# Optimization experiments

Hardware: AMD Instinct MI355X
Metric: run time of the kernel (lower is better)

## Reference

```python
import jax, jax.numpy as jnp
import numpy as np

B, Hdim, Wdim, C, NH, WS, SS = 8, 112, 112, 128, 4, 7, 3
N = WS * WS  # tokens per window


def _build_attn_mask(H, W, ws, ss):
    # standard Swin shifted-window mask: (nW, N, N) with 0 / -100
    img_mask = np.zeros((1, H, W, 1), dtype=np.float32)
    cnt = 0
    for h in (slice(0, -ws), slice(-ws, -ss), slice(-ss, None)):
        for w in (slice(0, -ws), slice(-ws, -ss), slice(-ss, None)):
            img_mask[:, h, w, :] = cnt
            cnt += 1
    mw = img_mask.reshape(1, H // ws, ws, W // ws, ws, 1)
    mw = mw.transpose(0, 1, 3, 2, 4, 5).reshape(-1, ws * ws)  # (nW, N)
    attn_mask = mw[:, None, :] - mw[:, :, None]
    return np.where(attn_mask != 0, np.float32(-100.0), np.float32(0.0))


def _rel_pos_index(ws):
    coords = np.stack(np.meshgrid(np.arange(ws), np.arange(ws), indexing='ij'))  # 2,ws,ws
    cf = coords.reshape(2, -1)
    rel = cf[:, :, None] - cf[:, None, :]  # 2,N,N
    rel = rel.transpose(1, 2, 0)
    rel[:, :, 0] += ws - 1
    rel[:, :, 1] += ws - 1
    rel[:, :, 0] *= 2 * ws - 1
    return rel.sum(-1).astype(np.int32)  # (N, N)


def setup_inputs() -> dict:
    key = jax.random.key(0)
    ks = jax.random.split(key, 6)
    x = jax.random.normal(ks[0], (B, Hdim * Wdim, C), dtype=jnp.float32)
    mask_matrix = jnp.asarray(_build_attn_mask(Hdim, Wdim, WS, SS))  # (256,49,49)
    s = 0.02
    qkv_w = jax.random.normal(ks[1], (3 * C, C), dtype=jnp.float32) * s
    qkv_b = jnp.zeros((3 * C,), dtype=jnp.float32)
    proj_w = jax.random.normal(ks[2], (C, C), dtype=jnp.float32) * s
    proj_b = jnp.zeros((C,), dtype=jnp.float32)
    rpb_table = jax.random.normal(ks[3], ((2 * WS - 1) ** 2, NH), dtype=jnp.float32) * s
    rel_index = jnp.asarray(_rel_pos_index(WS))
    return dict(x=x, mask_matrix=mask_matrix, qkv_w=qkv_w, qkv_b=qkv_b,
                proj_w=proj_w, proj_b=proj_b, rpb_table=rpb_table,
                rel_index=rel_index, H=Hdim, W=Wdim,
                window_size=WS, shift_size=SS, num_heads=NH)


def reference(x, mask_matrix, qkv_w, qkv_b, proj_w, proj_b, rpb_table,
              rel_index, H, W, window_size, shift_size, num_heads):
    Bb, L, Cc = x.shape
    ws, ss, nh = window_size, shift_size, num_heads
    hd = Cc // nh
    n = ws * ws
    x = x.reshape(Bb, H, W, Cc)
    if ss > 0:
        x = jnp.roll(x, shift=(-ss, -ss), axis=(1, 2))
    # window partition -> (Bb*nW, n, C)
    nWh, nWw = H // ws, W // ws
    xw = x.reshape(Bb, nWh, ws, nWw, ws, Cc).transpose(0, 1, 3, 2, 4, 5)
    xw = xw.reshape(-1, n, Cc)
    Bw = xw.shape[0]
    # qkv
    qkv = xw @ qkv_w.T + qkv_b  # (Bw, n, 3C)
    qkv = qkv.reshape(Bw, n, 3, nh, hd).transpose(2, 0, 3, 1, 4)
    q, k, v = qkv[0], qkv[1], qkv[2]  # (Bw, nh, n, hd)
    attn = jnp.einsum('bhnd,bhmd->bhnm', q * (hd ** -0.5), k)
    bias = rpb_table[rel_index.reshape(-1)].reshape(n, n, nh).transpose(2, 0, 1)
    attn = attn + bias[None]
    if ss > 0:
        nW = mask_matrix.shape[0]
        attn = attn.reshape(Bw // nW, nW, nh, n, n) + mask_matrix[None, :, None]
        attn = attn.reshape(Bw, nh, n, n)
    attn = jax.nn.softmax(attn, axis=-1)
    out = jnp.einsum('bhnm,bhmd->bhnd', attn, v)
    out = out.transpose(0, 2, 1, 3).reshape(Bw, n, Cc)
    out = out @ proj_w.T + proj_b
    # window reverse
    out = out.reshape(Bb, nWh, nWw, ws, ws, Cc).transpose(0, 1, 3, 2, 4, 5)
    out = out.reshape(Bb, H, W, Cc)
    if ss > 0:
        out = jnp.roll(out, shift=(ss, ss), axis=(1, 2))
    return out.reshape(Bb, H * W, Cc)
```

## Files before the change

### kernel.cpp

```cpp
#include <hip/hip_runtime.h>
#include <hip/hip_bf16.h>

typedef unsigned short u16;
typedef unsigned int   u32;
typedef __attribute__((ext_vector_type(8))) short bf16x8;
typedef __attribute__((ext_vector_type(4))) float f32x4;

__device__ __forceinline__ float bflo(u32 w) { return __uint_as_float(w << 16); }
__device__ __forceinline__ float bfhi(u32 w) { return __uint_as_float(w & 0xffff0000u); }
__device__ __forceinline__ u16 f2bf(float f) {
    u32 u = __float_as_uint(f);
    return (u16)((u + 0x7fffu + ((u >> 16) & 1u)) >> 16);
}
__device__ __forceinline__ u32 pk2(float lo, float hi) {
    union { __hip_bfloat162 h; u32 u; } cvt;
    cvt.h = __float22bfloat162_rn(make_float2(lo, hi));
    return cvt.u;
}

constexpr int QK_STR = 40;
constexpr int VT_STR = 72;
constexpr int PW_STR = 72;
constexpr int XS_STR = 136;

__global__ void prep_kernel(const float* __restrict__ qkv_w,
                            const float* __restrict__ proj_w,
                            const float* __restrict__ mask,
                            const float* __restrict__ rpb,
                            const int*   __restrict__ rel,
                            u16* __restrict__ ws,
                            uint2* __restrict__ ftab)
{
    int i = blockIdx.x * 256 + threadIdx.x;
    if (i < 49152) {
        float v = qkv_w[i];
        if (i < 16384) v *= 0.17677669529663687f;
        ws[i] = f2bf(v);
    }
    if (i < 16384) ws[49152 + i] = f2bf(proj_w[i]);
    if (i < 16384) {
        int lane = i & 63, e = i >> 6;
        int nt = e & 3, mt = (e >> 2) & 3, h = (e >> 4) & 3, cls = e >> 6;
        int lr = lane & 15, lg = lane >> 4;
        int col = nt * 16 + lr;
        int rep = ((cls & 2) ? 240 : 0) + ((cls & 1) ? 15 : 0);
        float vj[4];
#pragma unroll
        for (int j = 0; j < 4; ++j) {
            int row = mt * 16 + lg * 4 + j;
            float val;
            if (col >= 49)      val = -30000.f;
            else if (row >= 49) val = 0.f;
            else val = rpb[rel[row * 49 + col] * 4 + h] + mask[(rep * 49 + row) * 49 + col];
            vj[j] = val;
        }
        uint2 pk;
        pk.x = (u32)f2bf(vj[0]) | ((u32)f2bf(vj[1]) << 16);
        pk.y = (u32)f2bf(vj[2]) | ((u32)f2bf(vj[3]) << 16);
        ftab[i] = pk;
    }
}

__global__ __launch_bounds__(512, 4)
void swin_mfma(const float* __restrict__ x,
               const float* __restrict__ qkv_b,
               const float* __restrict__ proj_b,
               const u16*   __restrict__ wqkv,
               const u16*   __restrict__ wproj,
               const uint2* __restrict__ ft2,
               float* __restrict__ out)
{
    __shared__ __align__(16) u16 q_s[4 * 64 * QK_STR];
    __shared__ __align__(16) u16 k_s[4 * 64 * QK_STR];
    __shared__ __align__(16) u16 vT_s[4 * 32 * VT_STR];
    __shared__ __align__(16) u16 pB[8 * 16 * PW_STR];
    u16* const xs = pB;

    const int tid  = threadIdx.x;
    const int w    = tid >> 6;
    const int lane = tid & 63;
    const int lr   = lane & 15;
    const int lg   = lane >> 4;
    const int bid  = blockIdx.x;
    const int b    = bid >> 8;
    const int wi   = bid & 255;
    const int wh   = wi >> 4, ww = wi & 15;
    const int cls  = ((wh == 15) ? 2 : 0) | ((ww == 15) ? 1 : 0);

    const int mt = w & 3;
    const int hp = w >> 2;

    for (int idx = tid; idx < 49 * 32; idx += 512) {
        int t = idx >> 5, c4 = (idx & 31) << 2;
        int tr = t / 7, tc = t - tr * 7;
        int hs = wh * 7 + tr + 3; if (hs >= 112) hs -= 112;
        int cs = ww * 7 + tc + 3; if (cs >= 112) cs -= 112;
        float4 xv = *(const float4*)&x[((b * 112 + hs) * 112 + cs) * 128 + c4];
        *(uint2*)&xs[t * XS_STR + c4] = make_uint2(pk2(xv.x, xv.y), pk2(xv.z, xv.w));
    }
    __syncthreads();

    bf16x8 a[4][4];
#pragma unroll
    for (int mt2 = 0; mt2 < 4; ++mt2) {
        bool valid = (mt2 * 16 + lr) < 49;
#pragma unroll
        for (int kt = 0; kt < 4; ++kt) {
            bf16x8 f = {0, 0, 0, 0, 0, 0, 0, 0};
            if (valid)
                f = *(const bf16x8*)&xs[(mt2 * 16 + lr) * XS_STR + kt * 32 + lg * 8];
            a[mt2][kt] = f;
        }
    }
#pragma unroll
    for (int mt2 = 0; mt2 < 4; ++mt2)
#pragma unroll
        for (int kt = 0; kt < 4; ++kt)
            asm volatile("" : "+v"(a[mt2][kt]));

#pragma unroll
    for (int t = 0; t < 3; ++t) {
        int n0 = w * 48 + t * 16;
        bf16x8 bw[4];
#pragma unroll
        for (int kt = 0; kt < 4; ++kt)
            bw[kt] = *(const bf16x8*)&wqkv[(n0 + lr) * 128 + kt * 32 + lg * 8];
        float bias = qkv_b[n0 + lr];
        int which = n0 >> 7;
        if (which == 0) bias *= 0.17677669529663687f;
        int h = (n0 & 127) >> 5;
        int d = (n0 & 31) + lr;
        f32x4 ci = {bias, bias, bias, bias};
#pragma unroll
        for (int mt2 = 0; mt2 < 4; ++mt2) {
            f32x4 acc = ci;
#pragma unroll
            for (int kt = 0; kt < 4; ++kt)
                acc = __builtin_amdgcn_mfma_f32_16x16x32_bf16(a[mt2][kt], bw[kt], acc, 0, 0, 0);
            u32 r01 = pk2(acc[0], acc[1]);
            u32 r23 = pk2(acc[2], acc[3]);
            if (which == 2) {
                *(uint2*)&vT_s[(h * 32 + d) * VT_STR + mt2 * 16 + lg * 4] =
                    make_uint2(r01, r23);
            } else {
                u16* dst = (which == 0) ? q_s : k_s;
                int rb = (h * 64 + mt2 * 16 + lg * 4) * QK_STR + d;
                dst[rb]              = (u16)r01;
                dst[rb + QK_STR]     = (u16)(r01 >> 16);
                dst[rb + 2 * QK_STR] = (u16)r23;
                dst[rb + 3 * QK_STR] = (u16)(r23 >> 16);
            }
        }
    }
    __syncthreads();

    float  invs[2][4];
    bf16x8 ap[2][2];
    u16* const pw = pB + w * 16 * PW_STR;
#pragma unroll
    for (int hl = 0; hl < 2; ++hl) {
        int h = hp * 2 + hl;
        bf16x8 aq = *(const bf16x8*)&q_s[(h * 64 + mt * 16 + lr) * QK_STR + lg * 8];
        int eb = ((cls * 4 + h) * 4 + mt) * 4;
        f32x4 sc[4];
#pragma unroll
        for (int nt = 0; nt < 4; ++nt) {
            bf16x8 bk = *(const bf16x8*)&k_s[(h * 64 + nt * 16 + lr) * QK_STR + lg * 8];
            uint2 cv = ft2[(eb + nt) * 64 + lane];
            f32x4 ci = {bflo(cv.x), bfhi(cv.x), bflo(cv.y), bfhi(cv.y)};
            sc[nt] = __builtin_amdgcn_mfma_f32_16x16x32_bf16(aq, bk, ci, 0, 0, 0);
        }
#pragma unroll
        for (int j = 0; j < 4; ++j) {
            float p0 = __expf(sc[0][j]), p1 = __expf(sc[1][j]);
            float p2 = __expf(sc[2][j]), p3 = __expf(sc[3][j]);
            float sm = (p0 + p1) + (p2 + p3);
            sm += __shfl_xor(sm, 1);
            sm += __shfl_xor(sm, 2);
            sm += __shfl_xor(sm, 4);
            sm += __shfl_xor(sm, 8);
            invs[hl][j] = 1.f / sm;
            u32 r01 = pk2(p0, p1), r23 = pk2(p2, p3);
            u16* pr = pw + (lg * 4 + j) * PW_STR;
            pr[lr]      = (u16)r01;
            pr[lr + 16] = (u16)(r01 >> 16);
            pr[lr + 32] = (u16)r23;
            pr[lr + 48] = (u16)(r23 >> 16);
        }
        ap[hl][0] = *(const bf16x8*)&pw[lr * PW_STR + lg * 8];
        ap[hl][1] = *(const bf16x8*)&pw[lr * PW_STR + 32 + lg * 8];
    }
#pragma unroll
    for (int hl = 0; hl < 2; ++hl) {
        int h = hp * 2 + hl;
#pragma unroll
        for (int nt = 0; nt < 2; ++nt) {
            bf16x8 bv0 = *(const bf16x8*)&vT_s[(h * 32 + nt * 16 + lr) * VT_STR + lg * 8];
            bf16x8 bv1 = *(const bf16x8*)&vT_s[(h * 32 + nt * 16 + lr) * VT_STR + 32 + lg * 8];
            f32x4 z = {0.f, 0.f, 0.f, 0.f};
            f32x4 o = __builtin_amdgcn_mfma_f32_16x16x32_bf16(ap[hl][0], bv0, z, 0, 0, 0);
            o = __builtin_amdgcn_mfma_f32_16x16x32_bf16(ap[hl][1], bv1, o, 0, 0, 0);
            u32 r01 = pk2(o[0] * invs[hl][0], o[1] * invs[hl][1]);
            u32 r23 = pk2(o[2] * invs[hl][2], o[3] * invs[hl][3]);
            int cbase = hl * 32 + nt * 16 + lr;
            pw[(lg * 4 + 0) * PW_STR + cbase] = (u16)r01;
            pw[(lg * 4 + 1) * PW_STR + cbase] = (u16)(r01 >> 16);
            pw[(lg * 4 + 2) * PW_STR + cbase] = (u16)r23;
            pw[(lg * 4 + 3) * PW_STR + cbase] = (u16)(r23 >> 16);
        }
    }
    __syncthreads();

    bf16x8 ao[4];
#pragma unroll
    for (int kt = 0; kt < 4; ++kt) {
        int srcw = (kt >> 1) * 4 + mt;
        ao[kt] = *(const bf16x8*)&pB[(srcw * 16 + lr) * PW_STR + (kt & 1) * 32 + lg * 8];
    }
    int obase[4];
#pragma unroll
    for (int j = 0; j < 4; ++j) {
        int tok = mt * 16 + lg * 4 + j;
        if (tok < 49) {
            int tr = tok / 7, tc = tok - tr * 7;
            int hs = wh * 7 + tr + 3; if (hs >= 112) hs -= 112;
            int cs = ww * 7 + tc + 3; if (cs >= 112) cs -= 112;
            obase[j] = ((b * 112 + hs) * 112 + cs) * 128;
        } else obase[j] = -1;
    }
#pragma unroll
    for (int tn = 0; tn < 4; ++tn) {
        int n0 = (hp * 4 + tn) * 16;
        bf16x8 bw[4];
#pragma unroll
        for (int kt = 0; kt < 4; ++kt)
            bw[kt] = *(const bf16x8*)&wproj[(n0 + lr) * 128 + kt * 32 + lg * 8];
        float bias = proj_b[n0 + lr];
        f32x4 acc = {bias, bias, bias, bias};
#pragma unroll
        for (int kt = 0; kt < 4; ++kt)
            acc = __builtin_amdgcn_mfma_f32_16x16x32_bf16(ao[kt], bw[kt], acc, 0, 0, 0);
#pragma unroll
        for (int j = 0; j < 4; ++j)
            if (obase[j] >= 0) out[obase[j] + n0 + lr] = acc[j];
    }
}

extern "C" void kernel_launch(void* const* d_in, const int* in_sizes, int n_in,
                              void* d_out, int out_size, void* d_ws, size_t ws_size,
                              hipStream_t stream) {
    (void)in_sizes; (void)n_in; (void)out_size; (void)ws_size;
    const float* x      = (const float*)d_in[0];
    const float* mask   = (const float*)d_in[1];
    const float* qkv_w  = (const float*)d_in[2];
    const float* qkv_b  = (const float*)d_in[3];
    const float* proj_w = (const float*)d_in[4];
    const float* proj_b = (const float*)d_in[5];
    const float* rpb    = (const float*)d_in[6];
    const int*   rel    = (const int*)d_in[7];
    float* out = (float*)d_out;

    u16*   ws16 = (u16*)d_ws;
    uint2* ftab = (uint2*)(ws16 + 65536);

    prep_kernel<<<dim3(192), dim3(256), 0, stream>>>(qkv_w, proj_w, mask, rpb, rel, ws16, ftab);
    swin_mfma<<<dim3(2048), dim3(512), 0, stream>>>(
        x, qkv_b, proj_b, ws16, ws16 + 49152, ftab, out);
}
```

Baseline: 78.43 us.

## Use exp2 with log2e-prescaled scores, MFMA row sums, prefetched bias table

Folds log2(e) into the Q weight/bias scale and the precomputed bias+mask table so the softmax can use exp2f instead of __expf. The row-sum reduction via four cross-lane shuffles per row is replaced with two MFMAs against a ones vector operating on the bf16 probabilities. The per-window bias/mask table loads are moved ahead of the first barrier so their latency overlaps the x staging, and an asm register pin on the A fragments is removed. Sums now come from bf16-rounded probabilities, which matches what is fed to the PV product but changes rounding slightly, and the prefetch holds extra registers across the QKV phase.

```diff
diff --git a/kernel.cpp b/kernel.cpp
--- a/kernel.cpp
+++ b/kernel.cpp
@@ -22,6 +22,9 @@
 constexpr int VT_STR = 72;
 constexpr int PW_STR = 72;
 constexpr int XS_STR = 136;
+
+constexpr float LOG2E   = 1.4426950408889634f;
+constexpr float QSCALE2 = 0.25503172931836417f;
 
 __global__ void prep_kernel(const float* __restrict__ qkv_w,
                             const float* __restrict__ proj_w,
@@ -34,7 +37,7 @@
     int i = blockIdx.x * 256 + threadIdx.x;
     if (i < 49152) {
         float v = qkv_w[i];
-        if (i < 16384) v *= 0.17677669529663687f;
+        if (i < 16384) v *= QSCALE2;
         ws[i] = f2bf(v);
     }
     if (i < 16384) ws[49152 + i] = f2bf(proj_w[i]);
@@ -52,7 +55,7 @@
             if (col >= 49)      val = -30000.f;
             else if (row >= 49) val = 0.f;
             else val = rpb[rel[row * 49 + col] * 4 + h] + mask[(rep * 49 + row) * 49 + col];
-            vj[j] = val;
+            vj[j] = val * LOG2E;
         }
         uint2 pk;
         pk.x = (u32)f2bf(vj[0]) | ((u32)f2bf(vj[1]) << 16);
@@ -98,6 +101,15 @@
         float4 xv = *(const float4*)&x[((b * 112 + hs) * 112 + cs) * 128 + c4];
         *(uint2*)&xs[t * XS_STR + c4] = make_uint2(pk2(xv.x, xv.y), pk2(xv.z, xv.w));
     }
+
+    uint2 cvv[2][4];
+#pragma unroll
+    for (int hl = 0; hl < 2; ++hl) {
+        int eb = ((cls * 4 + (hp * 2 + hl)) * 4 + mt) * 4;
+#pragma unroll
+        for (int nt = 0; nt < 4; ++nt)
+            cvv[hl][nt] = ft2[(eb + nt) * 64 + lane];
+    }
     __syncthreads();
 
     bf16x8 a[4][4];
@@ -112,11 +124,6 @@
             a[mt2][kt] = f;
         }
     }
-#pragma unroll
-    for (int mt2 = 0; mt2 < 4; ++mt2)
-#pragma unroll
-        for (int kt = 0; kt < 4; ++kt)
-            asm volatile("" : "+v"(a[mt2][kt]));
 
 #pragma unroll
     for (int t = 0; t < 3; ++t) {
@@ -127,7 +134,7 @@
             bw[kt] = *(const bf16x8*)&wqkv[(n0 + lr) * 128 + kt * 32 + lg * 8];
         float bias = qkv_b[n0 + lr];
         int which = n0 >> 7;
-        if (which == 0) bias *= 0.17677669529663687f;
+        if (which == 0) bias *= QSCALE2;
         int h = (n0 & 127) >> 5;
         int d = (n0 & 31) + lr;
         f32x4 ci = {bias, bias, bias, bias};
@@ -154,6 +161,8 @@
     }
     __syncthreads();
 
+    const short ONE = (short)0x3F80;
+    const bf16x8 ones = {ONE, ONE, ONE, ONE, ONE, ONE, ONE, ONE};
     float  invs[2][4];
     bf16x8 ap[2][2];
     u16* const pw = pB + w * 16 * PW_STR;
@@ -161,25 +170,18 @@
     for (int hl = 0; hl < 2; ++hl) {
         int h = hp * 2 + hl;
         bf16x8 aq = *(const bf16x8*)&q_s[(h * 64 + mt * 16 + lr) * QK_STR + lg * 8];
-        int eb = ((cls * 4 + h) * 4 + mt) * 4;
         f32x4 sc[4];
 #pragma unroll
         for (int nt = 0; nt < 4; ++nt) {
             bf16x8 bk = *(const bf16x8*)&k_s[(h * 64 + nt * 16 + lr) * QK_STR + lg * 8];
-            uint2 cv = ft2[(eb + nt) * 64 + lane];
+            uint2 cv = cvv[hl][nt];
             f32x4 ci = {bflo(cv.x), bfhi(cv.x), bflo(cv.y), bfhi(cv.y)};
             sc[nt] = __builtin_amdgcn_mfma_f32_16x16x32_bf16(aq, bk, ci, 0, 0, 0);
         }
 #pragma unroll
         for (int j = 0; j < 4; ++j) {
-            float p0 = __expf(sc[0][j]), p1 = __expf(sc[1][j]);
-            float p2 = __expf(sc[2][j]), p3 = __expf(sc[3][j]);
-            float sm = (p0 + p1) + (p2 + p3);
-            sm += __shfl_xor(sm, 1);
-            sm += __shfl_xor(sm, 2);
-            sm += __shfl_xor(sm, 4);
-            sm += __shfl_xor(sm, 8);
-            invs[hl][j] = 1.f / sm;
+            float p0 = exp2f(sc[0][j]), p1 = exp2f(sc[1][j]);
+            float p2 = exp2f(sc[2][j]), p3 = exp2f(sc[3][j]);
             u32 r01 = pk2(p0, p1), r23 = pk2(p2, p3);
             u16* pr = pw + (lg * 4 + j) * PW_STR;
             pr[lr]      = (u16)r01;
@@ -189,6 +191,12 @@
         }
         ap[hl][0] = *(const bf16x8*)&pw[lr * PW_STR + lg * 8];
         ap[hl][1] = *(const bf16x8*)&pw[lr * PW_STR + 32 + lg * 8];
+        f32x4 z = {0.f, 0.f, 0.f, 0.f};
+        f32x4 sums = __builtin_amdgcn_mfma_f32_16x16x32_bf16(ap[hl][0], ones, z, 0, 0, 0);
+        sums = __builtin_amdgcn_mfma_f32_16x16x32_bf16(ap[hl][1], ones, sums, 0, 0, 0);
+#pragma unroll
+        for (int j = 0; j < 4; ++j)
+            invs[hl][j] = 1.f / sums[j];
     }
 #pragma unroll
     for (int hl = 0; hl < 2; ++hl) {
```

After: 79.85 us. Within noise of the previous version (+1.8%).
